# Kernel tuning notes

Measured on AMD Instinct MI355X. Metric: run time of the kernel, lower is better.

Reference implementation:

```python
import jax, jax.numpy as jnp
import numpy as np

B, C, N, K, C_OUT = 4, 64, 8192, 16, 64


def setup_inputs() -> dict:
    key = jax.random.key(0)
    k1, k2, k3, k4 = jax.random.split(key, 4)
    x = jax.random.normal(k1, (B, C, N, 1), dtype=jnp.float32)
    edge_index = jax.random.randint(k2, (2, B, N, K), 0, N, dtype=jnp.int64)
    # 1x1 conv weights of BasicConv([2C, C_OUT]) -> [C_OUT, 2C]
    W = jax.random.normal(k3, (C_OUT, 2 * C), dtype=jnp.float32) * (1.0 / np.sqrt(2 * C))
    b = jax.random.normal(k4, (C_OUT,), dtype=jnp.float32) * 0.01
    return {"x": x, "edge_index": edge_index, "W": W, "b": b}


def _batched_index_select(x, idx):
    # x: [B, C, N] ; idx: [B, N, K] -> [B, C, N, K]
    b, c, n = x.shape
    k = idx.shape[-1]
    flat = jnp.broadcast_to(idx.reshape(b, 1, n * k), (b, c, n * k))
    return jnp.take_along_axis(x, flat, axis=2).reshape(b, c, n, k)


def reference(x, edge_index, W, b):
    xs = x[..., 0]                                  # [B, C, N]
    x_i = _batched_index_select(xs, edge_index[1])  # [B, C, N, K] central nodes
    x_j = _batched_index_select(xs, edge_index[0])  # [B, C, N, K] neighbors
    feat = jnp.concatenate([x_i, x_j - x_i], axis=1)  # [B, 2C, N, K]
    # 1x1 conv: [C_OUT, 2C] x [B, 2C, N, K] -> [B, C_OUT, N, K], + bias, ReLU (norm=None)
    h = jnp.einsum('oc,bcnk->bonk', W, feat) + b[None, :, None, None]
    h = jax.nn.relu(h)
    # max over neighbors, keepdim on last axis -> [B, C_OUT, N, 1]
    return jnp.max(h, axis=-1, keepdims=True)
```

## Files before the change

### kernel.cpp

```cpp
#include <hip/hip_runtime.h>


#define BB   4
#define CCH  64
#define NN   8192
#define KK   16

typedef _Float16 h2 __attribute__((ext_vector_type(2)));
typedef _Float16 h4 __attribute__((ext_vector_type(4)));

__global__ __launch_bounds__(256) void gemm_kernel(const float* __restrict__ x,
                                                   const float* __restrict__ W,
                                                   _Float16* __restrict__ y) {
    __shared__ float wT[64 * 132];
    __shared__ float xs[64 * 64];

    const int t   = threadIdx.x;
    const int blk = blockIdx.x;
    const int xcd  = blk & 7;
    const int b    = xcd >> 1;
    const int tile = ((blk >> 3) << 1) | (xcd & 1);
    const int n0   = tile * 64;

    {
        const int sbase = t >> 6;
        const int k     = t & 63;
        #pragma unroll
        for (int i = 0; i < 32; ++i) {
            const int s = sbase + (i << 2);
            float v;
            if (s < CCH) v = W[s * 128 + k] - W[s * 128 + 64 + k];
            else         v = W[(s - CCH) * 128 + 64 + k];
            wT[k * 132 + s] = v;
        }
    }
    {
        const float* xb = x + (size_t)b * CCH * NN + n0;
        #pragma unroll
        for (int i = 0; i < 16; ++i) {
            const int e = t + (i << 8);
            const int k = e >> 6, n = e & 63;
            xs[k * 64 + n] = xb[(size_t)k * NN + n];
        }
    }
    __syncthreads();

    const int c_grp = t & 31;
    const int n_grp = t >> 5;

    float acc[4][8];
    #pragma unroll
    for (int i = 0; i < 4; ++i)
        #pragma unroll
        for (int j = 0; j < 8; ++j) acc[i][j] = 0.f;

    #pragma unroll 8
    for (int k = 0; k < 64; ++k) {
        const float4 wv  = *(const float4*)&wT[k * 132 + 4 * c_grp];
        const float4 xv0 = *(const float4*)&xs[k * 64 + 8 * n_grp];
        const float4 xv1 = *(const float4*)&xs[k * 64 + 8 * n_grp + 4];
        const float wa[4] = {wv.x, wv.y, wv.z, wv.w};
        const float xa[8] = {xv0.x, xv0.y, xv0.z, xv0.w, xv1.x, xv1.y, xv1.z, xv1.w};
        #pragma unroll
        for (int i = 0; i < 4; ++i)
            #pragma unroll
            for (int j = 0; j < 8; ++j)
                acc[i][j] += wa[i] * xa[j];
    }

    _Float16* ybp = y + ((size_t)b * NN + n0) * 128 + 4 * c_grp;
    #pragma unroll
    for (int j = 0; j < 8; ++j) {
        h4 v;
        v.x = (_Float16)acc[0][j]; v.y = (_Float16)acc[1][j];
        v.z = (_Float16)acc[2][j]; v.w = (_Float16)acc[3][j];
        *(h4*)&ybp[(size_t)(8 * n_grp + j) * 128] = v;
    }
}

__global__ __launch_bounds__(256) void gather_kernel(const _Float16* __restrict__ y,
                                                     const int* __restrict__ edge,
                                                     const float* __restrict__ bias,
                                                     float* __restrict__ out) {
    __shared__ int   eL[16][2][16];
    __shared__ float so[16][65];

    const int t   = threadIdx.x;
    const int blk = blockIdx.x;
    const int xcd  = blk & 7;
    const int b    = xcd >> 1;
    const int tile = ((blk >> 3) << 1) | (xcd & 1);
    const int n0   = tile * 16;

    if (t < 128) {
        const int src = t >> 6;
        const int f   = (t & 63) << 2;
        const int nl  = f >> 4, k0 = f & 15;
        const size_t eb = (size_t)(src == 0 ? BB + b : b) * NN * KK;
        *(int4*)&eL[nl][src][k0] = *(const int4*)&edge[eb + (size_t)(n0 + nl) * KK + k0];
    }
    __syncthreads();

    const int w    = t >> 6;
    const int lane = t & 63;
    const int half = lane >> 5;
    const int cl   = lane & 31;

    const float2 bv = *(const float2*)&bias[2 * cl];
    const _Float16* yb = y + (size_t)b * NN * 128;

    #pragma unroll 2
    for (int u = 0; u < 4; ++u) {
        const int nl = 4 * w + u;
        h2 s[8];
        #pragma unroll
        for (int kp = 0; kp < 8; ++kp) {
            const int k  = 2 * kp + half;
            const int i1 = eL[nl][0][k];
            const int i0 = eL[nl][1][k];
            const uint a = *(const uint*)&yb[(size_t)i1 * 128 + 2 * cl];
            const uint c = *(const uint*)&yb[(size_t)i0 * 128 + 64 + 2 * cl];
            union { uint u32; h2 h; } ua, uc;
            ua.u32 = a; uc.u32 = c;
            s[kp] = ua.h + uc.h;
        }
        h2 m = s[0];
        #pragma unroll
        for (int kp = 1; kp < 8; ++kp) m = __builtin_elementwise_max(m, s[kp]);
        union { int i32; h2 h; } um, uo;
        um.h = m;
        uo.i32 = __shfl_xor(um.i32, 32, 64);
        m = __builtin_elementwise_max(m, uo.h);
        if (half == 0) {
            float2 r;
            r.x = fmaxf((float)m.x + bv.x, 0.f);
            r.y = fmaxf((float)m.y + bv.y, 0.f);
            *(float2*)&so[nl][2 * cl] = r;
        }
    }
    __syncthreads();

    {
        const int c = t >> 2;
        const int q = t & 3;
        float4 v;
        v.x = so[4 * q + 0][c];
        v.y = so[4 * q + 1][c];
        v.z = so[4 * q + 2][c];
        v.w = so[4 * q + 3][c];
        *(float4*)(out + ((size_t)b * CCH + c) * NN + n0 + 4 * q) = v;
    }
}

extern "C" void kernel_launch(void* const* d_in, const int* in_sizes, int n_in,
                              void* d_out, int out_size, void* d_ws, size_t ws_size,
                              hipStream_t stream) {
    (void)in_sizes; (void)n_in; (void)out_size; (void)ws_size;
    const float* x    = (const float*)d_in[0];
    const int*   edge = (const int*)d_in[1];
    const float* W    = (const float*)d_in[2];
    const float* bias = (const float*)d_in[3];
    float*       out  = (float*)d_out;
    _Float16*    y    = (_Float16*)d_ws;

    gemm_kernel<<<dim3(512), dim3(256), 0, stream>>>(x, W, y);
    gather_kernel<<<dim3(2048), dim3(256), 0, stream>>>(y, edge, bias, out);
}
```

Before: 27.99 us.

## Use fp16 packed dot products in the GEMM with larger 128x128 tiles

```diff
diff --git a/kernel.cpp b/kernel.cpp
--- a/kernel.cpp
+++ b/kernel.cpp
@@ -6,75 +6,88 @@
 #define NN   8192
 #define KK   16
 
-typedef _Float16 h2 __attribute__((ext_vector_type(2)));
-typedef _Float16 h4 __attribute__((ext_vector_type(4)));
+typedef _Float16 h2  __attribute__((ext_vector_type(2)));
+typedef _Float16 h8  __attribute__((ext_vector_type(8)));
+typedef _Float16 h16 __attribute__((ext_vector_type(16)));
+typedef int      v4i __attribute__((ext_vector_type(4)));
+
+#if __has_builtin(__builtin_amdgcn_fdot2)
+#define FDOT2(a, b, c) __builtin_amdgcn_fdot2((a), (b), (c), false)
+#else
+#define FDOT2(a, b, c) ((c) + (float)(a).x * (float)(b).x + (float)(a).y * (float)(b).y)
+#endif
 
 __global__ __launch_bounds__(256) void gemm_kernel(const float* __restrict__ x,
                                                    const float* __restrict__ W,
                                                    _Float16* __restrict__ y) {
-    __shared__ float wT[64 * 132];
-    __shared__ float xs[64 * 64];
+    __shared__ _Float16 wT2[32 * 264];
+    __shared__ _Float16 xs2[32 * 264];
 
     const int t   = threadIdx.x;
     const int blk = blockIdx.x;
-    const int xcd  = blk & 7;
-    const int b    = xcd >> 1;
-    const int tile = ((blk >> 3) << 1) | (xcd & 1);
-    const int n0   = tile * 64;
+    const int b   = blk >> 6;
+    const int n0  = (blk & 63) * 128;
 
     {
-        const int sbase = t >> 6;
-        const int k     = t & 63;
+        const int k  = t & 63;
+        const int kp = k >> 1, par = k & 1;
+        const int sb = t >> 6;
         #pragma unroll
         for (int i = 0; i < 32; ++i) {
-            const int s = sbase + (i << 2);
+            const int s = sb + 4 * i;
             float v;
             if (s < CCH) v = W[s * 128 + k] - W[s * 128 + 64 + k];
             else         v = W[(s - CCH) * 128 + 64 + k];
-            wT[k * 132 + s] = v;
+            wT2[kp * 264 + 2 * s + par] = (_Float16)v;
         }
     }
     {
         const float* xb = x + (size_t)b * CCH * NN + n0;
         #pragma unroll
-        for (int i = 0; i < 16; ++i) {
-            const int e = t + (i << 8);
-            const int k = e >> 6, n = e & 63;
-            xs[k * 64 + n] = xb[(size_t)k * NN + n];
+        for (int i = 0; i < 8; ++i) {
+            const int k  = (t >> 5) + 8 * i;
+            const int nq = (t & 31) * 4;
+            const float4 v = *(const float4*)&xb[(size_t)k * NN + nq];
+            const int kp = k >> 1, par = k & 1;
+            _Float16* d = &xs2[kp * 264 + 2 * nq + par];
+            d[0] = (_Float16)v.x; d[2] = (_Float16)v.y;
+            d[4] = (_Float16)v.z; d[6] = (_Float16)v.w;
         }
     }
     __syncthreads();
 
-    const int c_grp = t & 31;
-    const int n_grp = t >> 5;
+    const int sg = t & 15;
+    const int ng = t >> 4;
+    const int s0 = sg * 8, nn0 = ng * 8;
 
-    float acc[4][8];
+    float acc[8][8];
     #pragma unroll
-    for (int i = 0; i < 4; ++i)
+    for (int i = 0; i < 8; ++i)
         #pragma unroll
         for (int j = 0; j < 8; ++j) acc[i][j] = 0.f;
 
-    #pragma unroll 8
-    for (int k = 0; k < 64; ++k) {
-        const float4 wv  = *(const float4*)&wT[k * 132 + 4 * c_grp];
-        const float4 xv0 = *(const float4*)&xs[k * 64 + 8 * n_grp];
-        const float4 xv1 = *(const float4*)&xs[k * 64 + 8 * n_grp + 4];
-        const float wa[4] = {wv.x, wv.y, wv.z, wv.w};
-        const float xa[8] = {xv0.x, xv0.y, xv0.z, xv0.w, xv1.x, xv1.y, xv1.z, xv1.w};
+    #pragma unroll 2
+    for (int kp = 0; kp < 32; ++kp) {
+        const h16 wv = *(const h16*)&wT2[kp * 264 + 2 * s0];
+        const h16 xv = *(const h16*)&xs2[kp * 264 + 2 * nn0];
         #pragma unroll
-        for (int i = 0; i < 4; ++i)
+        for (int i = 0; i < 8; ++i) {
+            h2 wp; wp.x = wv[2 * i]; wp.y = wv[2 * i + 1];
             #pragma unroll
-            for (int j = 0; j < 8; ++j)
-                acc[i][j] += wa[i] * xa[j];
+            for (int j = 0; j < 8; ++j) {
+                h2 xp; xp.x = xv[2 * j]; xp.y = xv[2 * j + 1];
+                acc[i][j] = FDOT2(wp, xp, acc[i][j]);
+            }
+        }
     }
 
-    _Float16* ybp = y + ((size_t)b * NN + n0) * 128 + 4 * c_grp;
+    _Float16* yb = y + ((size_t)b * NN + n0 + nn0) * 128 + s0;
     #pragma unroll
     for (int j = 0; j < 8; ++j) {
-        h4 v;
-        v.x = (_Float16)acc[0][j]; v.y = (_Float16)acc[1][j];
-        v.z = (_Float16)acc[2][j]; v.w = (_Float16)acc[3][j];
-        *(h4*)&ybp[(size_t)(8 * n_grp + j) * 128] = v;
+        h8 v;
+        #pragma unroll
+        for (int i = 0; i < 8; ++i) v[i] = (_Float16)acc[i][j];
+        *(h8*)&yb[(size_t)j * 128] = v;
     }
 }
 
@@ -97,7 +110,7 @@
         const int f   = (t & 63) << 2;
         const int nl  = f >> 4, k0 = f & 15;
         const size_t eb = (size_t)(src == 0 ? BB + b : b) * NN * KK;
-        *(int4*)&eL[nl][src][k0] = *(const int4*)&edge[eb + (size_t)(n0 + nl) * KK + k0];
+        *(v4i*)&eL[nl][src][k0] = *(const v4i*)&edge[eb + (size_t)(n0 + nl) * KK + k0];
     }
     __syncthreads();
 
@@ -163,6 +176,6 @@
     float*       out  = (float*)d_out;
     _Float16*    y    = (_Float16*)d_ws;
 
-    gemm_kernel<<<dim3(512), dim3(256), 0, stream>>>(x, W, y);
+    gemm_kernel<<<dim3(256), dim3(256), 0, stream>>>(x, W, y);
     gather_kernel<<<dim3(2048), dim3(256), 0, stream>>>(y, edge, bias, out);
 }
```

After: 27.20 us. 1.03x faster.
